# Optimization experiments

Measured on AMD Instinct MI355X. Metric: run time of the kernel, lower is better.

The kernel has to match this reference:

```python
import jax, jax.numpy as jnp
from jax import lax
import numpy as np

BS, HID, INP, NSPAN, NOUT, NUM_DAYS = 4096, 1024, 512, 8, 2, 20


def setup_inputs() -> dict:
    key = jax.random.key(0)
    ks = jax.random.split(key, 12)
    s = 1.0 / np.sqrt(HID)  # torch default uniform(-1/sqrt(hid), 1/sqrt(hid))
    u = lambda k, shape: jax.random.uniform(k, shape, jnp.float32, -s, s)
    return {
        "hx": jax.random.normal(ks[0], (BS, HID), jnp.float32),
        "cx": jax.random.normal(ks[1], (BS, HID), jnp.float32),
        "W_ih": u(ks[2], (4 * HID, INP)),
        "W_hh": u(ks[3], (4 * HID, HID)),
        "b_ih": u(ks[4], (4 * HID,)),
        "b_hh": u(ks[5], (4 * HID,)),
        "W_fcin": u(ks[6], (INP, HID)),
        "b_fcin": u(ks[7], (INP,)),
        "W_fcout": u(ks[8], (NOUT, HID)),
        "b_fcout": u(ks[9], (NOUT,)),
        "W_span": u(ks[10], (NSPAN, HID)),
        "b_span": u(ks[11], (NSPAN,)),
    }


def reference(hx, cx, W_ih, W_hh, b_ih, b_hh, W_fcin, b_fcin, W_fcout, b_fcout, W_span, b_span):
    # num-span head on the initial hidden state
    num_spans = jax.nn.softmax(hx @ W_span.T + b_span, axis=-1)  # [B, NSPAN]

    def step(carry, _):
        h, c, inp = carry
        gates = inp @ W_ih.T + b_ih + h @ W_hh.T + b_hh  # [B, 4H]
        i, f, g, o = jnp.split(gates, 4, axis=-1)  # torch LSTMCell gate order i,f,g,o
        c = jax.nn.sigmoid(f) * c + jax.nn.sigmoid(i) * jnp.tanh(g)
        h = jax.nn.sigmoid(o) * jnp.tanh(c)
        inp = jax.nn.relu(h @ W_fcin.T + b_fcin)  # next-step input
        out = jax.nn.softmax(h @ W_fcout.T + b_fcout, axis=-1)  # [B, 2]
        return (h, c, inp), out

    inp0 = jnp.zeros((hx.shape[0], W_ih.shape[1]), hx.dtype)
    _, outs = lax.scan(step, (hx, cx, inp0), None, length=NUM_DAYS)  # [T, B, 2]
    outputs = jnp.transpose(outs, (1, 0, 2))  # [B, T, 2]
    return num_spans, outputs
```

## Files before the change

### kernel.cpp

```cpp
#include <hip/hip_runtime.h>

typedef __bf16 bf16x8 __attribute__((ext_vector_type(8)));
typedef float f32x4 __attribute__((ext_vector_type(4)));
typedef unsigned short ushort_t;
typedef unsigned short u16x8 __attribute__((ext_vector_type(8)));

#define BSZ 4096
#define HID 1024
#define INPD 512
#define NSPAN 8
#define NOUT 2
#define NDAYS 20
#define XLD 1536


__device__ __forceinline__ ushort_t f2bf(float f) {
  union { float f; unsigned u; } v; v.f = f;
  unsigned r = v.u + 0x7FFFu + ((v.u >> 16) & 1u);
  return (ushort_t)(r >> 16);
}
__device__ __forceinline__ float bf2f(ushort_t b) {
  union { unsigned u; float f; } v; v.u = ((unsigned)b) << 16;
  return v.f;
}
__device__ __forceinline__ float sigf(float x) { return 1.f / (1.f + __expf(-x)); }
__device__ __forceinline__ float tanhfast(float x) { return 2.f / (1.f + __expf(-2.f * x)) - 1.f; }

__device__ __forceinline__ void gload16(const void* g, void* l) {
  __builtin_amdgcn_global_load_lds((const __attribute__((address_space(1))) void*)g,
                                   (__attribute__((address_space(3))) void*)l, 16, 0, 0);
}

__global__ void prep_gates_w(const float* __restrict__ Wih, const float* __restrict__ Whh,
                             const float* __restrict__ bih, const float* __restrict__ bhh,
                             ushort_t* __restrict__ Wgf, float* __restrict__ bg) {
  int gid = blockIdx.x * 256 + threadIdx.x;
  int rb = gid / 3072;
  int rem = gid - rb * 3072;
  int kk = rem >> 6;
  int li = rem & 63;
  int rp = rb * 16 + (li & 15);
  int kb = kk * 32 + ((li >> 4) << 3);
  int g = (rp >> 4) & 3;
  int j = (rp >> 6) * 16 + (rp & 15);
  int src = g * HID + j;
  const float* s = (kb < INPD) ? (Wih + (size_t)src * INPD + kb)
                               : (Whh + (size_t)src * HID + (kb - INPD));
  u16x8 o;
#pragma unroll
  for (int e = 0; e < 8; ++e) o[e] = f2bf(s[e]);
  *(u16x8*)(Wgf + (size_t)gid * 8) = o;
  if (kk == 0 && li < 16) bg[rp] = bih[src] + bhh[src];
}

__global__ void prep_fcin_w(const float* __restrict__ W, const float* __restrict__ Wout,
                            ushort_t* __restrict__ Wf) {
  int gid = blockIdx.x * 256 + threadIdx.x;
  int rb = gid / 2048;
  int rem = gid - rb * 2048;
  int kk = rem >> 6;
  int li = rem & 63;
  int row = rb * 16 + (li & 15);
  int kb = kk * 32 + ((li >> 4) << 3);
  u16x8 o;
  if (row < 512) {
    const float* s = W + (size_t)row * HID + kb;
#pragma unroll
    for (int e = 0; e < 8; ++e) o[e] = f2bf(s[e]);
  } else if (row < 514) {
    const float* s = Wout + (size_t)(row - 512) * HID + kb;
#pragma unroll
    for (int e = 0; e < 8; ++e) o[e] = f2bf(s[e]);
  } else {
#pragma unroll
    for (int e = 0; e < 8; ++e) o[e] = 0;
  }
  *(u16x8*)(Wf + (size_t)gid * 8) = o;
}

__global__ void init_x(const float* __restrict__ hx, ushort_t* __restrict__ Xf) {
  int gid = blockIdx.x * 256 + threadIdx.x;
  int rb = gid / 3072;
  int rem = gid - rb * 3072;
  int kk = rem >> 6;
  int li = rem & 63;
  int row = rb * 16 + (li & 15);
  int kb = kk * 32 + ((li >> 4) << 3);
  u16x8 o;
  if (kb < INPD) {
#pragma unroll
    for (int e = 0; e < 8; ++e) o[e] = 0;
  } else {
    const float* s = hx + (size_t)row * HID + (kb - INPD);
#pragma unroll
    for (int e = 0; e < 8; ++e) o[e] = f2bf(s[e]);
  }
  *(u16x8*)(Xf + (size_t)gid * 8) = o;
}

__global__ void span_kernel(const float* __restrict__ hx, const float* __restrict__ Wspan,
                            const float* __restrict__ bspan, float* __restrict__ out) {
  int gid = blockIdx.x * 256 + threadIdx.x;
  int b = gid >> 3, o = gid & 7;
  const float4* hr = (const float4*)(hx + (size_t)b * HID);
  const float4* wr = (const float4*)(Wspan + (size_t)o * HID);
  float acc = 0.f;
  for (int i = 0; i < HID / 4; ++i) {
    float4 h = hr[i], w = wr[i];
    acc += h.x * w.x + h.y * w.y + h.z * w.z + h.w * w.w;
  }
  acc += bspan[o];
  float m = acc;
  for (int s = 1; s < 8; s <<= 1) m = fmaxf(m, __shfl_xor(m, s));
  float e = __expf(acc - m);
  float ssum = e;
  for (int s = 1; s < 8; s <<= 1) ssum += __shfl_xor(ssum, s);
  out[gid] = e / ssum;
}

__global__ void fcout_kernel(const ushort_t* __restrict__ Xf, const float* __restrict__ W,
                             const float* __restrict__ bvec, float* __restrict__ outp, int t) {
  const int lane = threadIdx.x & 63;
  const int wave = threadIdx.x >> 6;
  const int b = blockIdx.x * 4 + wave;
  const int rb = b >> 4, r = b & 15;
  const int kk = 16 + (lane >> 1);
  const int ss = (lane & 1) * 2;
  const size_t base = ((size_t)rb * 48 + kk) * 512 + (ss * 16 + r) * 8;
  u16x8 h0 = *(const u16x8*)(Xf + base);
  u16x8 h1 = *(const u16x8*)(Xf + base + 128);
  const float* w0 = W + lane * 16;
  const float* w1 = W + HID + lane * 16;
  float l0 = 0.f, l1 = 0.f;
#pragma unroll
  for (int j = 0; j < 8; ++j) {
    float ha = bf2f(h0[j]);
    l0 += ha * w0[j];
    l1 += ha * w1[j];
    float hb = bf2f(h1[j]);
    l0 += hb * w0[j + 8];
    l1 += hb * w1[j + 8];
  }
#pragma unroll
  for (int s = 32; s > 0; s >>= 1) {
    l0 += __shfl_xor(l0, s);
    l1 += __shfl_xor(l1, s);
  }
  if (lane == 0) {
    l0 += bvec[0];
    l1 += bvec[1];
    float m = fmaxf(l0, l1);
    float e0 = __expf(l0 - m), e1 = __expf(l1 - m);
    float inv = 1.f / (e0 + e1);
    float* o = outp + (size_t)b * (NDAYS * NOUT) + t * NOUT;
    o[0] = e0 * inv;
    o[1] = e1 * inv;
  }
}

__global__ void gates128_kernel(const ushort_t* __restrict__ A,
                                const ushort_t* __restrict__ B,
                                const float* __restrict__ bias, float* __restrict__ cbuf,
                                ushort_t* __restrict__ hout) {
  __shared__ __align__(16) ushort_t ldsA[8 * 512];
  __shared__ __align__(16) ushort_t ldsB[8 * 512];
  const int tid = threadIdx.x;
  const int lane = tid & 63;
  const int wave = tid >> 6;

  int bid = blockIdx.y * gridDim.x + blockIdx.x;
  int nwg = gridDim.x * gridDim.y;
  int cpx = nwg >> 3;
  int swz = (bid & 7) * cpx + (bid >> 3);
  int bx = swz % gridDim.x;
  int by = swz / gridDim.x;
  const int bm = bx * 128;
  const int bn = by * 128;
  const int wm = (wave >> 1) * 64;
  const int wn = (wave & 1) * 64;

  f32x4 acc[4][4] = {};

  const int f0 = wave * 2, f1 = wave * 2 + 1;
  const ushort_t* gA0 = A + ((size_t)((bm >> 4) + f0) * 48) * 512 + lane * 8;
  const ushort_t* gA1 = A + ((size_t)((bm >> 4) + f1) * 48) * 512 + lane * 8;
  const ushort_t* gB0 = B + ((size_t)((bn >> 4) + f0) * 48) * 512 + lane * 8;
  const ushort_t* gB1 = B + ((size_t)((bn >> 4) + f1) * 48) * 512 + lane * 8;

  for (int kk = 0; kk < 48; ++kk) {
    const int ko = kk * 512;
    gload16(gA0 + ko, ldsA + f0 * 512);
    gload16(gA1 + ko, ldsA + f1 * 512);
    gload16(gB0 + ko, ldsB + f0 * 512);
    gload16(gB1 + ko, ldsB + f1 * 512);
    __syncthreads();

    bf16x8 af[4], bf[4];
#pragma unroll
    for (int i = 0; i < 4; ++i) {
      af[i] = *(const bf16x8*)(ldsA + ((wm >> 4) + i) * 512 + lane * 8);
      bf[i] = *(const bf16x8*)(ldsB + ((wn >> 4) + i) * 512 + lane * 8);
    }
#pragma unroll
    for (int mi = 0; mi < 4; ++mi)
#pragma unroll
      for (int ni = 0; ni < 4; ++ni)
        acc[mi][ni] = __builtin_amdgcn_mfma_f32_16x16x32_bf16(af[mi], bf[ni], acc[mi][ni], 0, 0, 0);
    __syncthreads();
  }

  const int colbase = bn + wn;
  const int jj = (colbase >> 6) * 16 + (lane & 15);
  const int cb = colbase + (lane & 15);
  const float bI = bias[cb];
  const float bF = bias[cb + 16];
  const float bG = bias[cb + 32];
  const float bO = bias[cb + 48];
  const size_t kpart = (size_t)(16 + (jj >> 5)) * 512 + ((jj & 31) >> 3) * 128 + (jj & 7);
  const int q4 = (lane >> 4) << 2;
#pragma unroll
  for (int mi = 0; mi < 4; ++mi) {
    const size_t rowbase = (size_t)(((bm + wm) >> 4) + mi) * 24576 + kpart;
#pragma unroll
    for (int r = 0; r < 4; ++r) {
      const int b = bm + wm + mi * 16 + q4 + r;
      float ig = sigf(acc[mi][0][r] + bI);
      float fg = sigf(acc[mi][1][r] + bF);
      float gg = tanhfast(acc[mi][2][r] + bG);
      float og = sigf(acc[mi][3][r] + bO);
      size_t cidx = (size_t)b * HID + jj;
      float cn = fg * cbuf[cidx] + ig * gg;
      cbuf[cidx] = cn;
      hout[rowbase + (q4 + r) * 8] = f2bf(og * tanhfast(cn));
    }
  }
}

__global__ __launch_bounds__(256) void fcin_direct(
    const ushort_t* __restrict__ Xf, const ushort_t* __restrict__ Bw,
    const float* __restrict__ bias, ushort_t* __restrict__ hout,
    const float* __restrict__ bout, float* __restrict__ outp, int t) {
  const int tid = threadIdx.x;
  const int lane = tid & 63;
  const int wave = tid >> 6;
  const int bid = blockIdx.x;
  const int swz = (bid & 7) * 36 + (bid >> 3);
  const int wt = swz * 4 + wave;
  const int n_idx = wt >> 7;
  const int m_idx = wt & 127;

  const ushort_t* pA0 = Xf + (((size_t)(m_idx * 2 + 0) * 48 + 16) << 9) + lane * 8;
  const ushort_t* pA1 = Xf + (((size_t)(m_idx * 2 + 1) * 48 + 16) << 9) + lane * 8;
  const ushort_t* pB0 = Bw + (((size_t)(n_idx * 4 + 0) * 32) << 9) + lane * 8;
  const ushort_t* pB1 = Bw + (((size_t)(n_idx * 4 + 1) * 32) << 9) + lane * 8;
  const ushort_t* pB2 = Bw + (((size_t)(n_idx * 4 + 2) * 32) << 9) + lane * 8;
  const ushort_t* pB3 = Bw + (((size_t)(n_idx * 4 + 3) * 32) << 9) + lane * 8;

  f32x4 acc[2][4] = {};
  bf16x8 aC0, aC1, bC[4], aN0, aN1, bN[4];

  aC0 = *(const bf16x8*)(pA0);
  aC1 = *(const bf16x8*)(pA1);
  bC[0] = *(const bf16x8*)(pB0);
  bC[1] = *(const bf16x8*)(pB1);
  bC[2] = *(const bf16x8*)(pB2);
  bC[3] = *(const bf16x8*)(pB3);

#pragma unroll 2
  for (int kp = 0; kp < 16; ++kp) {
    const int o1 = (2 * kp + 1) << 9;
    aN0 = *(const bf16x8*)(pA0 + o1);
    aN1 = *(const bf16x8*)(pA1 + o1);
    bN[0] = *(const bf16x8*)(pB0 + o1);
    bN[1] = *(const bf16x8*)(pB1 + o1);
    bN[2] = *(const bf16x8*)(pB2 + o1);
    bN[3] = *(const bf16x8*)(pB3 + o1);
#pragma unroll
    for (int ni = 0; ni < 4; ++ni) {
      acc[0][ni] = __builtin_amdgcn_mfma_f32_16x16x32_bf16(aC0, bC[ni], acc[0][ni], 0, 0, 0);
      acc[1][ni] = __builtin_amdgcn_mfma_f32_16x16x32_bf16(aC1, bC[ni], acc[1][ni], 0, 0, 0);
    }
    if (kp < 15) {
      const int o2 = (2 * kp + 2) << 9;
      aC0 = *(const bf16x8*)(pA0 + o2);
      aC1 = *(const bf16x8*)(pA1 + o2);
      bC[0] = *(const bf16x8*)(pB0 + o2);
      bC[1] = *(const bf16x8*)(pB1 + o2);
      bC[2] = *(const bf16x8*)(pB2 + o2);
      bC[3] = *(const bf16x8*)(pB3 + o2);
    }
#pragma unroll
    for (int ni = 0; ni < 4; ++ni) {
      acc[0][ni] = __builtin_amdgcn_mfma_f32_16x16x32_bf16(aN0, bN[ni], acc[0][ni], 0, 0, 0);
      acc[1][ni] = __builtin_amdgcn_mfma_f32_16x16x32_bf16(aN1, bN[ni], acc[1][ni], 0, 0, 0);
    }
  }

  const int q4 = (lane >> 4) << 2;
  if (n_idx < 8) {
#pragma unroll
    for (int mi = 0; mi < 2; ++mi) {
      const size_t rowbase = (size_t)(m_idx * 2 + mi) * 24576;
#pragma unroll
      for (int ni = 0; ni < 4; ++ni) {
        const int n = n_idx * 64 + ni * 16 + (lane & 15);
        const float bb = bias[n];
        const size_t kpart = (size_t)(n >> 5) * 512 + ((n & 31) >> 3) * 128 + (n & 7);
#pragma unroll
        for (int r = 0; r < 4; ++r) {
          float v = fmaxf(acc[mi][ni][r] + bb, 0.f);
          hout[rowbase + kpart + (q4 + r) * 8] = f2bf(v);
        }
      }
    }
  } else {
    const float b0 = bout[0], b1 = bout[1];
#pragma unroll
    for (int mi = 0; mi < 2; ++mi) {
#pragma unroll
      for (int r = 0; r < 4; ++r) {
        float raw = acc[mi][0][r];
        float partner = __shfl_xor(raw, 1);
        if ((lane & 15) == 0) {
          float l0 = raw + b0;
          float l1 = partner + b1;
          float m = fmaxf(l0, l1);
          float e0 = __expf(l0 - m), e1 = __expf(l1 - m);
          float inv = 1.f / (e0 + e1);
          const int row = m_idx * 32 + mi * 16 + q4 + r;
          float* o = outp + (size_t)row * (NDAYS * NOUT) + t * NOUT;
          o[0] = e0 * inv;
          o[1] = e1 * inv;
        }
      }
    }
  }
}

extern "C" void kernel_launch(void* const* d_in, const int* in_sizes, int n_in, void* d_out,
                              int out_size, void* d_ws, size_t ws_size, hipStream_t stream) {
  const float* hx = (const float*)d_in[0];
  const float* cx = (const float*)d_in[1];
  const float* Wih = (const float*)d_in[2];
  const float* Whh = (const float*)d_in[3];
  const float* bih = (const float*)d_in[4];
  const float* bhh = (const float*)d_in[5];
  const float* Wfcin = (const float*)d_in[6];
  const float* bfcin = (const float*)d_in[7];
  const float* Wfcout = (const float*)d_in[8];
  const float* bfcout = (const float*)d_in[9];
  const float* Wspan = (const float*)d_in[10];
  const float* bspan = (const float*)d_in[11];
  float* out = (float*)d_out;

  char* ws = (char*)d_ws;
  ushort_t* Wgf = (ushort_t*)(ws);
  ushort_t* Wfc2 = (ushort_t*)(ws + 12582912);
  float* bg = (float*)(ws + 13762560);
  ushort_t* XA = (ushort_t*)(ws + 13778944);
  ushort_t* XB = (ushort_t*)(ws + 26361856);
  float* cbuf = (float*)(ws + 38944768);

  prep_gates_w<<<3072, 256, 0, stream>>>(Wih, Whh, bih, bhh, Wgf, bg);
  prep_fcin_w<<<288, 256, 0, stream>>>(Wfcin, Wfcout, Wfc2);
  init_x<<<3072, 256, 0, stream>>>(hx, XA);
  hipMemcpyAsync(cbuf, cx, (size_t)BSZ * HID * 4, hipMemcpyDeviceToDevice, stream);
  span_kernel<<<(BSZ * NSPAN) / 256, 256, 0, stream>>>(hx, Wspan, bspan, out);

  float* outp = out + BSZ * NSPAN;
  for (int t = 0; t < NDAYS; ++t) {
    ushort_t* Xin = (t & 1) ? XB : XA;
    ushort_t* Xout = (t & 1) ? XA : XB;
    gates128_kernel<<<dim3(32, 32), 256, 0, stream>>>(Xin, Wgf, bg, cbuf, Xout);
    if (t < NDAYS - 1) {
      fcin_direct<<<288, 256, 0, stream>>>(Xout, Wfc2, bfcin, Xout, bfcout, outp, t);
    } else {
      fcout_kernel<<<BSZ / 4, 256, 0, stream>>>(Xout, Wfcout, bfcout, outp, t);
    }
  }
}
```

Measured before the change: 1.515 ms.

## Use two waves per gates tile, each computing a 64x128 sub-tile

The gates GEMM block drops from four waves to two. Each wave now computes a 64x128 output sub-tile (4x8 MFMA accumulators), which doubles the MFMA work per LDS fragment load. Wave 0 loads all A fragments and wave 1 loads all B fragments, 8 loads each per k-step. This raises register pressure and leaves fewer waves to hide latency, mitigated by launch bounds of 128 threads with 2 blocks per SIMD target.

Measured after the change: 1.543 ms. About the same (+1.8%).

```diff
diff --git a/kernel.cpp b/kernel.cpp
--- a/kernel.cpp
+++ b/kernel.cpp
@@ -158,10 +158,10 @@
   }
 }
 
-__global__ void gates128_kernel(const ushort_t* __restrict__ A,
-                                const ushort_t* __restrict__ B,
-                                const float* __restrict__ bias, float* __restrict__ cbuf,
-                                ushort_t* __restrict__ hout) {
+__global__ __launch_bounds__(128, 2) void gates128_kernel(
+    const ushort_t* __restrict__ A, const ushort_t* __restrict__ B,
+    const float* __restrict__ bias, float* __restrict__ cbuf,
+    ushort_t* __restrict__ hout) {
   __shared__ __align__(16) ushort_t ldsA[8 * 512];
   __shared__ __align__(16) ushort_t ldsB[8 * 512];
   const int tid = threadIdx.x;
@@ -176,62 +176,63 @@
   int by = swz / gridDim.x;
   const int bm = bx * 128;
   const int bn = by * 128;
-  const int wm = (wave >> 1) * 64;
-  const int wn = (wave & 1) * 64;
-
-  f32x4 acc[4][4] = {};
-
-  const int f0 = wave * 2, f1 = wave * 2 + 1;
-  const ushort_t* gA0 = A + ((size_t)((bm >> 4) + f0) * 48) * 512 + lane * 8;
-  const ushort_t* gA1 = A + ((size_t)((bm >> 4) + f1) * 48) * 512 + lane * 8;
-  const ushort_t* gB0 = B + ((size_t)((bn >> 4) + f0) * 48) * 512 + lane * 8;
-  const ushort_t* gB1 = B + ((size_t)((bn >> 4) + f1) * 48) * 512 + lane * 8;
+  const int wm = wave * 64;
+
+  f32x4 acc[4][8] = {};
+
+  const ushort_t* gS = (wave == 0)
+      ? (A + ((size_t)(bm >> 4) * 48) * 512 + lane * 8)
+      : (B + ((size_t)(bn >> 4) * 48) * 512 + lane * 8);
+  ushort_t* lD = (wave == 0) ? ldsA : ldsB;
 
   for (int kk = 0; kk < 48; ++kk) {
-    const int ko = kk * 512;
-    gload16(gA0 + ko, ldsA + f0 * 512);
-    gload16(gA1 + ko, ldsA + f1 * 512);
-    gload16(gB0 + ko, ldsB + f0 * 512);
-    gload16(gB1 + ko, ldsB + f1 * 512);
+    const size_t ko = (size_t)kk * 512;
+#pragma unroll
+    for (int f = 0; f < 8; ++f)
+      gload16(gS + (size_t)f * 24576 + ko, lD + f * 512);
     __syncthreads();
 
-    bf16x8 af[4], bf[4];
-#pragma unroll
-    for (int i = 0; i < 4; ++i) {
-      af[i] = *(const bf16x8*)(ldsA + ((wm >> 4) + i) * 512 + lane * 8);
-      bf[i] = *(const bf16x8*)(ldsB + ((wn >> 4) + i) * 512 + lane * 8);
-    }
+    bf16x8 af[4], bf[8];
+#pragma unroll
+    for (int i = 0; i < 4; ++i)
+      af[i] = *(const bf16x8*)(ldsA + (wave * 4 + i) * 512 + lane * 8);
+#pragma unroll
+    for (int n = 0; n < 8; ++n)
+      bf[n] = *(const bf16x8*)(ldsB + n * 512 + lane * 8);
 #pragma unroll
     for (int mi = 0; mi < 4; ++mi)
 #pragma unroll
-      for (int ni = 0; ni < 4; ++ni)
+      for (int ni = 0; ni < 8; ++ni)
         acc[mi][ni] = __builtin_amdgcn_mfma_f32_16x16x32_bf16(af[mi], bf[ni], acc[mi][ni], 0, 0, 0);
     __syncthreads();
   }
 
-  const int colbase = bn + wn;
-  const int jj = (colbase >> 6) * 16 + (lane & 15);
-  const int cb = colbase + (lane & 15);
-  const float bI = bias[cb];
-  const float bF = bias[cb + 16];
-  const float bG = bias[cb + 32];
-  const float bO = bias[cb + 48];
-  const size_t kpart = (size_t)(16 + (jj >> 5)) * 512 + ((jj & 31) >> 3) * 128 + (jj & 7);
   const int q4 = (lane >> 4) << 2;
 #pragma unroll
-  for (int mi = 0; mi < 4; ++mi) {
-    const size_t rowbase = (size_t)(((bm + wm) >> 4) + mi) * 24576 + kpart;
-#pragma unroll
-    for (int r = 0; r < 4; ++r) {
-      const int b = bm + wm + mi * 16 + q4 + r;
-      float ig = sigf(acc[mi][0][r] + bI);
-      float fg = sigf(acc[mi][1][r] + bF);
-      float gg = tanhfast(acc[mi][2][r] + bG);
-      float og = sigf(acc[mi][3][r] + bO);
-      size_t cidx = (size_t)b * HID + jj;
-      float cn = fg * cbuf[cidx] + ig * gg;
-      cbuf[cidx] = cn;
-      hout[rowbase + (q4 + r) * 8] = f2bf(og * tanhfast(cn));
+  for (int g = 0; g < 2; ++g) {
+    const int colbase = bn + g * 64;
+    const int jj = (colbase >> 6) * 16 + (lane & 15);
+    const int cb = colbase + (lane & 15);
+    const float bI = bias[cb];
+    const float bF = bias[cb + 16];
+    const float bG = bias[cb + 32];
+    const float bO = bias[cb + 48];
+    const size_t kpart = (size_t)(16 + (jj >> 5)) * 512 + ((jj & 31) >> 3) * 128 + (jj & 7);
+#pragma unroll
+    for (int mi = 0; mi < 4; ++mi) {
+      const size_t rowbase = (size_t)(((bm + wm) >> 4) + mi) * 24576 + kpart;
+#pragma unroll
+      for (int r = 0; r < 4; ++r) {
+        const int b = bm + wm + mi * 16 + q4 + r;
+        float ig = sigf(acc[mi][g * 4 + 0][r] + bI);
+        float fg = sigf(acc[mi][g * 4 + 1][r] + bF);
+        float gg = tanhfast(acc[mi][g * 4 + 2][r] + bG);
+        float og = sigf(acc[mi][g * 4 + 3][r] + bO);
+        size_t cidx = (size_t)b * HID + jj;
+        float cn = fg * cbuf[cidx] + ig * gg;
+        cbuf[cidx] = cn;
+        hout[rowbase + (q4 + r) * 8] = f2bf(og * tanhfast(cn));
+      }
     }
   }
 }
@@ -371,7 +372,7 @@
   for (int t = 0; t < NDAYS; ++t) {
     ushort_t* Xin = (t & 1) ? XB : XA;
     ushort_t* Xout = (t & 1) ? XA : XB;
-    gates128_kernel<<<dim3(32, 32), 256, 0, stream>>>(Xin, Wgf, bg, cbuf, Xout);
+    gates128_kernel<<<dim3(32, 32), 128, 0, stream>>>(Xin, Wgf, bg, cbuf, Xout);
     if (t < NDAYS - 1) {
       fcin_direct<<<288, 256, 0, stream>>>(Xout, Wfc2, bfcin, Xout, bfcout, outp, t);
     } else {
```
